# Optimization experiments

Measured on AMD Instinct MI355X. Metric: run time of the kernel, lower is better.

Reference implementation:

```python
import jax, jax.numpy as jnp
import numpy as np

N_HEADS = 12
C = 3          # per-head in/hidden/out channels (12/4)
C_PRED = 1     # predictor hidden (4/4)
BN_EPS = 1e-5
COS_EPS = 1e-8
B, H, W = 8, 512, 768


def setup_inputs() -> dict:
    key = jax.random.key(0)
    ks = jax.random.split(key, 22)
    p = lambda k, s: jax.random.normal(k, s, jnp.float32) * 0.1
    return {
        "latent1": jax.random.normal(ks[0], (B, N_HEADS, H, W), jnp.float32),
        "latent2": jax.random.normal(ks[1], (B, N_HEADS, H, W), jnp.float32),
        # projector conv1 + BN
        "W1": p(ks[2], (N_HEADS, C, C)), "b1": p(ks[3], (N_HEADS, C)),
        "g1": 1.0 + p(ks[4], (N_HEADS, C)), "be1": p(ks[5], (N_HEADS, C)),
        # projector conv2 + BN
        "W2": p(ks[6], (N_HEADS, C, C)), "b2": p(ks[7], (N_HEADS, C)),
        "g2": 1.0 + p(ks[8], (N_HEADS, C)), "be2": p(ks[9], (N_HEADS, C)),
        # projector conv3 + BN (no ReLU)
        "W3": p(ks[10], (N_HEADS, C, C)), "b3": p(ks[11], (N_HEADS, C)),
        "g3": 1.0 + p(ks[12], (N_HEADS, C)), "be3": p(ks[13], (N_HEADS, C)),
        # predictor conv1 + BN
        "W4": p(ks[14], (N_HEADS, C_PRED, C)), "b4": p(ks[15], (N_HEADS, C_PRED)),
        "g4": 1.0 + p(ks[16], (N_HEADS, C_PRED)), "be4": p(ks[17], (N_HEADS, C_PRED)),
        # predictor conv2 (no BN)
        "W5": p(ks[18], (N_HEADS, C, C_PRED)), "b5": p(ks[19], (N_HEADS, C)),
    }


def _conv1x1(x, Wk, bk):
    # x: [B, Cin, H, W'], Wk: [Cout, Cin]
    return jnp.einsum('oc,bchw->bohw', Wk, x) + bk[None, :, None, None]


def _bn(x, g, be):
    # training-mode BatchNorm2d: batch statistics over (B, H, W)
    m = x.mean(axis=(0, 2, 3), keepdims=True)
    v = x.var(axis=(0, 2, 3), keepdims=True)  # biased var, as torch BN uses
    return (x - m) * jax.lax.rsqrt(v + BN_EPS) * g[None, :, None, None] + be[None, :, None, None]


def _cos_loss(p, z):
    # -mean(cosine_similarity(p, detach(z), dim=1))
    z = jax.lax.stop_gradient(z)
    dot = jnp.sum(p * z, axis=1)
    npn = jnp.maximum(jnp.sqrt(jnp.sum(p * p, axis=1)), COS_EPS)
    nzn = jnp.maximum(jnp.sqrt(jnp.sum(z * z, axis=1)), COS_EPS)
    return -jnp.mean(dot / (npn * nzn))


def _head_loss(x1, x2, W1, b1, g1, be1, W2, b2, g2, be2, W3, b3, g3, be3,
               W4, b4, g4, be4, W5, b5):
    def proj(x):
        x = jax.nn.relu(_bn(_conv1x1(x, W1, b1), g1, be1))
        x = jax.nn.relu(_bn(_conv1x1(x, W2, b2), g2, be2))
        return _bn(_conv1x1(x, W3, b3), g3, be3)

    def pred(z):
        h = jax.nn.relu(_bn(_conv1x1(z, W4, b4), g4, be4))
        return _conv1x1(h, W5, b5)

    z1, z2 = proj(x1), proj(x2)
    p1, p2 = pred(z1), pred(z2)
    return 0.5 * (_cos_loss(p1, z2) + _cos_loss(p2, z1))


def reference(latent1, latent2, W1, b1, g1, be1, W2, b2, g2, be2,
              W3, b3, g3, be3, W4, b4, g4, be4, W5, b5):
    Bd, Cd, Hd, Wd = latent1.shape
    Wp = Wd // C
    # per-channel view [B, H, W] -> [B, 3, H, W/3]; stack heads on leading axis
    x1 = latent1.reshape(Bd, N_HEADS, C, Hd, Wp).transpose(1, 0, 2, 3, 4)
    x2 = latent2.reshape(Bd, N_HEADS, C, Hd, Wp).transpose(1, 0, 2, 3, 4)
    losses = jax.vmap(_head_loss)(x1, x2, W1, b1, g1, be1, W2, b2, g2, be2,
                                  W3, b3, g3, be3, W4, b4, g4, be4, W5, b5)
    return jnp.sum(losses)
```

## Files before the change

### kernel.cpp

```cpp
#include <hip/hip_runtime.h>
#include <math.h>


typedef unsigned short ushort_t;
typedef unsigned int uint_t;

constexpr int   NH      = 12;
constexpr int   POS     = 131072;
constexpr int   NB      = 8;
constexpr long long MLL = (long long)NB * POS;
constexpr int   CSPAN   = POS / 16;
constexpr int   SBLK    = 128;
constexpr int   NTOT    = NB * NH * 3 * POS;
constexpr float COS_EPS = 1e-8f;

constexpr size_t XB_BYTES   = (size_t)NTOT * 2;
constexpr size_t DBL_COUNT  = (size_t)24 * SBLK * 9 + (size_t)24 * SBLK * 6 +
                              (size_t)24 * SBLK * 9 + (size_t)12 * SBLK;
constexpr size_t NEED_BYTES = 2 * XB_BYTES + DBL_COUNT * 8 + 480 * 4;

template <int K>
__device__ inline void block_reduce_to0(double (&v)[K]) {
#pragma unroll
  for (int off = 32; off > 0; off >>= 1) {
#pragma unroll
    for (int k = 0; k < K; ++k) v[k] += __shfl_down(v[k], off, 64);
  }
  __shared__ double lds[4][K];
  const int lane = threadIdx.x & 63;
  const int wv   = threadIdx.x >> 6;
  if (lane == 0) {
#pragma unroll
    for (int k = 0; k < K; ++k) lds[wv][k] = v[k];
  }
  __syncthreads();
  if (threadIdx.x == 0) {
#pragma unroll
    for (int k = 0; k < K; ++k) v[k] = lds[0][k] + lds[1][k] + lds[2][k] + lds[3][k];
  }
}

__device__ inline uint_t pack2bf(float lo, float hi) {
  uint_t ul = __float_as_uint(lo);
  uint_t uh = __float_as_uint(hi);
  ul = ul + 0x7FFFu + ((ul >> 16) & 1u);
  uh = uh + 0x7FFFu + ((uh >> 16) & 1u);
  return (ul >> 16) | (uh & 0xFFFF0000u);
}

__device__ inline void unpack8(const uint4 v, float (&f)[8]) {
  const uint_t w0 = v.x, w1 = v.y, w2 = v.z, w3 = v.w;
  f[0] = __uint_as_float(w0 << 16); f[1] = __uint_as_float(w0 & 0xFFFF0000u);
  f[2] = __uint_as_float(w1 << 16); f[3] = __uint_as_float(w1 & 0xFFFF0000u);
  f[4] = __uint_as_float(w2 << 16); f[5] = __uint_as_float(w2 & 0xFFFF0000u);
  f[6] = __uint_as_float(w3 << 16); f[7] = __uint_as_float(w3 & 0xFFFF0000u);
}

template <bool BF16>
__device__ inline void load_ch3(const float* __restrict__ X,
                                const ushort_t* __restrict__ XB,
                                size_t eoff, float (&f)[3][8]) {
#pragma unroll
  for (int c = 0; c < 3; ++c) {
    const size_t a = eoff + (size_t)c * POS;
    if constexpr (BF16) {
      const uint4 v = *(const uint4*)(XB + a);
      unpack8(v, f[c]);
    } else {
      const float4 u0 = *(const float4*)(X + a);
      const float4 u1 = *(const float4*)(X + a + 4);
      f[c][0] = u0.x; f[c][1] = u0.y; f[c][2] = u0.z; f[c][3] = u0.w;
      f[c][4] = u1.x; f[c][5] = u1.y; f[c][6] = u1.z; f[c][7] = u1.w;
    }
  }
}

template <bool STORE>
__global__ __launch_bounds__(256) void passA_kernel(
    const float* __restrict__ x1, const float* __restrict__ x2,
    ushort_t* __restrict__ xb1, ushort_t* __restrict__ xb2,
    double* __restrict__ P0) {
  const int u = blockIdx.y;
  const int s = u % 24;
  const int b = u / 24;
  const int n = s >> 1;
  const float* __restrict__ X = (s & 1) ? x2 : x1;
  ushort_t* __restrict__ XB = (s & 1) ? xb2 : xb1;
  const size_t off0 = (size_t)((b * NH + n) * 3) * POS + (size_t)blockIdx.x * CSPAN;

  float acc[9] = {0.f, 0.f, 0.f, 0.f, 0.f, 0.f, 0.f, 0.f, 0.f};
#pragma unroll
  for (int i = 0; i < 8; ++i) {
    const int idx = i * 1024 + threadIdx.x * 4;
    float4 v[3];
#pragma unroll
    for (int c = 0; c < 3; ++c)
      v[c] = *(const float4*)(X + off0 + (size_t)c * POS + idx);
    if constexpr (STORE) {
#pragma unroll
      for (int c = 0; c < 3; ++c) {
        uint2 h;
        h.x = pack2bf(v[c].x, v[c].y);
        h.y = pack2bf(v[c].z, v[c].w);
        *(uint2*)(XB + off0 + (size_t)c * POS + idx) = h;
      }
    }
    const float* f0 = (const float*)&v[0];
    const float* f1 = (const float*)&v[1];
    const float* f2 = (const float*)&v[2];
#pragma unroll
    for (int j = 0; j < 4; ++j) {
      const float X0 = f0[j], X1 = f1[j], X2 = f2[j];
      acc[0] += X0;      acc[1] += X1;      acc[2] += X2;
      acc[3] += X0 * X0; acc[4] += X1 * X1; acc[5] += X2 * X2;
      acc[6] += X0 * X1; acc[7] += X0 * X2; acc[8] += X1 * X2;
    }
  }

  double v9[9];
#pragma unroll
  for (int k = 0; k < 9; ++k) v9[k] = (double)acc[k];
  block_reduce_to0<9>(v9);
  if (threadIdx.x == 0) {
    double* dst = P0 + ((size_t)s * SBLK + b * 16 + blockIdx.x) * 9;
#pragma unroll
    for (int k = 0; k < 9; ++k) dst[k] = v9[k];
  }
}

__global__ __launch_bounds__(256) void bn_statsA_kernel(
    const double* __restrict__ P0, const float* __restrict__ W1,
    const float* __restrict__ b1, const float* __restrict__ g1,
    const float* __restrict__ be1, float* __restrict__ derived) {
  const int s = blockIdx.x;
  const int t = threadIdx.x;
  const int n = s >> 1;
  double v[9] = {0, 0, 0, 0, 0, 0, 0, 0, 0};
  if (t < SBLK) {
    const double* p = P0 + ((size_t)s * SBLK + t) * 9;
#pragma unroll
    for (int k = 0; k < 9; ++k) v[k] = p[k];
  }
  block_reduce_to0<9>(v);
  if (t == 0) {
    const double M = (double)MLL;
    double m[3] = {v[0] / M, v[1] / M, v[2] / M};
    double C00 = v[3] / M - m[0] * m[0];
    double C11 = v[4] / M - m[1] * m[1];
    double C22 = v[5] / M - m[2] * m[2];
    double C01 = v[6] / M - m[0] * m[1];
    double C02 = v[7] / M - m[0] * m[2];
    double C12 = v[8] / M - m[1] * m[2];
    for (int o = 0; o < 3; ++o) {
      const double w0 = W1[n * 9 + o * 3 + 0];
      const double w1v = W1[n * 9 + o * 3 + 1];
      const double w2v = W1[n * 9 + o * 3 + 2];
      const double my = w0 * m[0] + w1v * m[1] + w2v * m[2] + (double)b1[n * 3 + o];
      const double vy = w0 * w0 * C00 + w1v * w1v * C11 + w2v * w2v * C22 +
                        2.0 * (w0 * w1v * C01 + w0 * w2v * C02 + w1v * w2v * C12);
      const double sc = (double)g1[n * 3 + o] / sqrt(vy + 1e-5);
      derived[s * 20 + o]     = (float)sc;
      derived[s * 20 + 3 + o] = (float)((double)be1[n * 3 + o] - my * sc);
    }
  }
}

template <bool BF16>
__global__ __launch_bounds__(256) void passB_kernel(
    const float* __restrict__ x1, const float* __restrict__ x2,
    const ushort_t* __restrict__ xb1, const ushort_t* __restrict__ xb2,
    const float* __restrict__ W1, const float* __restrict__ b1,
    const float* __restrict__ W2, const float* __restrict__ b2,
    const float* __restrict__ derived, double* __restrict__ P2) {
  const int u = blockIdx.y;
  const int s = u % 24;
  const int b = u / 24;
  const int n = s >> 1;
  const float* __restrict__ X = (s & 1) ? x2 : x1;
  const ushort_t* __restrict__ XB = (s & 1) ? xb2 : xb1;
  const size_t off0 = (size_t)((b * NH + n) * 3) * POS + (size_t)blockIdx.x * CSPAN;

  float w1[3][3], bb1[3], w2[3][3], bb2[3], s1[3], t1[3];
#pragma unroll
  for (int o = 0; o < 3; ++o) {
#pragma unroll
    for (int c = 0; c < 3; ++c) {
      w1[o][c] = W1[n * 9 + o * 3 + c];
      w2[o][c] = W2[n * 9 + o * 3 + c];
    }
    bb1[o] = b1[n * 3 + o];
    bb2[o] = b2[n * 3 + o];
    s1[o]  = derived[s * 20 + o];
    t1[o]  = derived[s * 20 + 3 + o];
  }

  float acc[6] = {0.f, 0.f, 0.f, 0.f, 0.f, 0.f};
#pragma unroll 2
  for (int i = 0; i < 4; ++i) {
    const size_t eoff = off0 + i * 2048 + threadIdx.x * 8;
    float f[3][8];
    load_ch3<BF16>(X, XB, eoff, f);
#pragma unroll
    for (int j = 0; j < 8; ++j) {
      const float X0 = f[0][j], X1 = f[1][j], X2 = f[2][j];
      float a[3];
#pragma unroll
      for (int o = 0; o < 3; ++o) {
        const float y = fmaf(w1[o][0], X0, fmaf(w1[o][1], X1, fmaf(w1[o][2], X2, bb1[o])));
        a[o] = fmaxf(0.f, fmaf(s1[o], y, t1[o]));
      }
#pragma unroll
      for (int o = 0; o < 3; ++o) {
        const float y2v = fmaf(w2[o][0], a[0], fmaf(w2[o][1], a[1], fmaf(w2[o][2], a[2], bb2[o])));
        acc[o]     += y2v;
        acc[3 + o] += y2v * y2v;
      }
    }
  }

  double v[6];
#pragma unroll
  for (int k = 0; k < 6; ++k) v[k] = (double)acc[k];
  block_reduce_to0<6>(v);
  if (threadIdx.x == 0) {
    double* dst = P2 + ((size_t)s * SBLK + b * 16 + blockIdx.x) * 6;
#pragma unroll
    for (int k = 0; k < 6; ++k) dst[k] = v[k];
  }
}

__global__ __launch_bounds__(256) void bn_statsB_kernel(
    const double* __restrict__ P2, const float* __restrict__ gamma,
    const float* __restrict__ beta, float* __restrict__ derived) {
  const int s = blockIdx.x;
  const int t = threadIdx.x;
  const int n = s >> 1;
  double v[6] = {0, 0, 0, 0, 0, 0};
  if (t < SBLK) {
    const double* p = P2 + ((size_t)s * SBLK + t) * 6;
#pragma unroll
    for (int k = 0; k < 6; ++k) v[k] = p[k];
  }
  block_reduce_to0<6>(v);
  if (t == 0) {
#pragma unroll
    for (int c = 0; c < 3; ++c) {
      const double mean = v[c] / (double)MLL;
      const double var  = v[3 + c] / (double)MLL - mean * mean;
      const double sc   = (double)gamma[n * 3 + c] / sqrt(var + 1e-5);
      derived[s * 20 + 6 + c] = (float)sc;
      derived[s * 20 + 9 + c] = (float)((double)beta[n * 3 + c] - mean * sc);
    }
  }
}

template <bool BF16>
__global__ __launch_bounds__(256) void passC_kernel(
    const float* __restrict__ x1, const float* __restrict__ x2,
    const ushort_t* __restrict__ xb1, const ushort_t* __restrict__ xb2,
    const float* __restrict__ W1, const float* __restrict__ b1,
    const float* __restrict__ W2, const float* __restrict__ b2,
    const float* __restrict__ W3, const float* __restrict__ b3,
    const float* __restrict__ derived, double* __restrict__ P3) {
  const int u = blockIdx.y;
  const int s = u % 24;
  const int b = u / 24;
  const int n = s >> 1;
  const float* __restrict__ X = (s & 1) ? x2 : x1;
  const ushort_t* __restrict__ XB = (s & 1) ? xb2 : xb1;
  const size_t off0 = (size_t)((b * NH + n) * 3) * POS + (size_t)blockIdx.x * CSPAN;

  float w1[3][3], bb1[3], w2[3][3], bb2[3], w3[3][3], bb3[3];
  float s1[3], t1[3], s2[3], t2[3];
#pragma unroll
  for (int o = 0; o < 3; ++o) {
#pragma unroll
    for (int c = 0; c < 3; ++c) {
      w1[o][c] = W1[n * 9 + o * 3 + c];
      w2[o][c] = W2[n * 9 + o * 3 + c];
      w3[o][c] = W3[n * 9 + o * 3 + c];
    }
    bb1[o] = b1[n * 3 + o];
    bb2[o] = b2[n * 3 + o];
    bb3[o] = b3[n * 3 + o];
    s1[o]  = derived[s * 20 + o];
    t1[o]  = derived[s * 20 + 3 + o];
    s2[o]  = derived[s * 20 + 6 + o];
    t2[o]  = derived[s * 20 + 9 + o];
  }

  float acc[9] = {0.f, 0.f, 0.f, 0.f, 0.f, 0.f, 0.f, 0.f, 0.f};
#pragma unroll 2
  for (int i = 0; i < 4; ++i) {
    const size_t eoff = off0 + i * 2048 + threadIdx.x * 8;
    float f[3][8];
    load_ch3<BF16>(X, XB, eoff, f);
#pragma unroll
    for (int j = 0; j < 8; ++j) {
      const float X0 = f[0][j], X1 = f[1][j], X2 = f[2][j];
      float a[3], a2[3], y3[3];
#pragma unroll
      for (int o = 0; o < 3; ++o) {
        const float y = fmaf(w1[o][0], X0, fmaf(w1[o][1], X1, fmaf(w1[o][2], X2, bb1[o])));
        a[o] = fmaxf(0.f, fmaf(s1[o], y, t1[o]));
      }
#pragma unroll
      for (int o = 0; o < 3; ++o) {
        const float y = fmaf(w2[o][0], a[0], fmaf(w2[o][1], a[1], fmaf(w2[o][2], a[2], bb2[o])));
        a2[o] = fmaxf(0.f, fmaf(s2[o], y, t2[o]));
      }
#pragma unroll
      for (int o = 0; o < 3; ++o) {
        y3[o] = fmaf(w3[o][0], a2[0], fmaf(w3[o][1], a2[1], fmaf(w3[o][2], a2[2], bb3[o])));
        acc[o]     += y3[o];
        acc[3 + o] += y3[o] * y3[o];
      }
      acc[6] += y3[0] * y3[1];
      acc[7] += y3[0] * y3[2];
      acc[8] += y3[1] * y3[2];
    }
  }

  double v[9];
#pragma unroll
  for (int k = 0; k < 9; ++k) v[k] = (double)acc[k];
  block_reduce_to0<9>(v);
  if (threadIdx.x == 0) {
    double* dst = P3 + ((size_t)s * SBLK + b * 16 + blockIdx.x) * 9;
#pragma unroll
    for (int k = 0; k < 9; ++k) dst[k] = v[k];
  }
}

__global__ __launch_bounds__(256) void bn_statsC_kernel(
    const double* __restrict__ P3, const float* __restrict__ g3,
    const float* __restrict__ be3, const float* __restrict__ W4,
    const float* __restrict__ b4, const float* __restrict__ g4,
    const float* __restrict__ be4, float* __restrict__ derived) {
  const int s = blockIdx.x;
  const int t = threadIdx.x;
  const int n = s >> 1;
  double v[9] = {0, 0, 0, 0, 0, 0, 0, 0, 0};
  if (t < SBLK) {
    const double* p = P3 + ((size_t)s * SBLK + t) * 9;
#pragma unroll
    for (int k = 0; k < 9; ++k) v[k] = p[k];
  }
  block_reduce_to0<9>(v);
  if (t == 0) {
    const double M = (double)MLL;
    double mean[3] = {v[0] / M, v[1] / M, v[2] / M};
    double cov[3][3];
    cov[0][0] = v[3] / M - mean[0] * mean[0];
    cov[1][1] = v[4] / M - mean[1] * mean[1];
    cov[2][2] = v[5] / M - mean[2] * mean[2];
    cov[0][1] = cov[1][0] = v[6] / M - mean[0] * mean[1];
    cov[0][2] = cov[2][0] = v[7] / M - mean[0] * mean[2];
    cov[1][2] = cov[2][1] = v[8] / M - mean[1] * mean[2];

    double s3[3], t3[3];
    for (int c = 0; c < 3; ++c) {
      s3[c] = (double)g3[n * 3 + c] / sqrt(cov[c][c] + 1e-5);
      t3[c] = (double)be3[n * 3 + c] - mean[c] * s3[c];
      derived[s * 20 + 12 + c] = (float)s3[c];
      derived[s * 20 + 15 + c] = (float)t3[c];
    }
    double u[3], dd = (double)b4[n];
    for (int c = 0; c < 3; ++c) {
      u[c] = (double)W4[n * 3 + c] * s3[c];
      dd += (double)W4[n * 3 + c] * t3[c];
    }
    double m4 = dd;
    for (int c = 0; c < 3; ++c) m4 += u[c] * mean[c];
    double v4 = 0.0;
    for (int i = 0; i < 3; ++i)
      for (int j = 0; j < 3; ++j) v4 += u[i] * u[j] * cov[i][j];
    const double s4 = (double)g4[n] / sqrt(v4 + 1e-5);
    derived[s * 20 + 18] = (float)s4;
    derived[s * 20 + 19] = (float)((double)be4[n] - m4 * s4);
  }
}

__device__ inline void fwd_chain(
    const float w1[3][3], const float bb1[3],
    const float w2[3][3], const float bb2[3],
    const float w3[3][3], const float bb3[3],
    const float w4[3], float b4s, const float w5[3], const float b5v[3],
    const float* S, float X0, float X1, float X2, float z[3], float p[3]) {
  float a[3], a2[3];
#pragma unroll
  for (int o = 0; o < 3; ++o) {
    const float y = fmaf(w1[o][0], X0, fmaf(w1[o][1], X1, fmaf(w1[o][2], X2, bb1[o])));
    a[o] = fmaxf(0.f, fmaf(S[o], y, S[3 + o]));
  }
#pragma unroll
  for (int o = 0; o < 3; ++o) {
    const float y = fmaf(w2[o][0], a[0], fmaf(w2[o][1], a[1], fmaf(w2[o][2], a[2], bb2[o])));
    a2[o] = fmaxf(0.f, fmaf(S[6 + o], y, S[9 + o]));
  }
  float y4 = b4s;
#pragma unroll
  for (int o = 0; o < 3; ++o) {
    const float y = fmaf(w3[o][0], a2[0], fmaf(w3[o][1], a2[1], fmaf(w3[o][2], a2[2], bb3[o])));
    z[o] = fmaf(S[12 + o], y, S[15 + o]);
    y4 = fmaf(w4[o], z[o], y4);
  }
  const float h = fmaxf(0.f, fmaf(S[18], y4, S[19]));
#pragma unroll
  for (int o = 0; o < 3; ++o) p[o] = fmaf(w5[o], h, b5v[o]);
}

template <bool BF16>
__global__ __launch_bounds__(256) void passD_kernel(
    const float* __restrict__ x1, const float* __restrict__ x2,
    const ushort_t* __restrict__ xb1, const ushort_t* __restrict__ xb2,
    const float* __restrict__ W1, const float* __restrict__ b1,
    const float* __restrict__ W2, const float* __restrict__ b2,
    const float* __restrict__ W3, const float* __restrict__ b3,
    const float* __restrict__ W4, const float* __restrict__ b4,
    const float* __restrict__ W5, const float* __restrict__ b5,
    const float* __restrict__ derived, double* __restrict__ PL) {
  const int u = blockIdx.y;
  const int n = u % 12;
  const int b = u / 12;
  const size_t off0 = (size_t)((b * NH + n) * 3) * POS + (size_t)blockIdx.x * CSPAN;

  float w1[3][3], bb1[3], w2[3][3], bb2[3], w3[3][3], bb3[3];
  float w4[3], b4s, w5[3], b5v[3];
#pragma unroll
  for (int o = 0; o < 3; ++o) {
#pragma unroll
    for (int c = 0; c < 3; ++c) {
      w1[o][c] = W1[n * 9 + o * 3 + c];
      w2[o][c] = W2[n * 9 + o * 3 + c];
      w3[o][c] = W3[n * 9 + o * 3 + c];
    }
    bb1[o] = b1[n * 3 + o];
    bb2[o] = b2[n * 3 + o];
    bb3[o] = b3[n * 3 + o];
    w4[o]  = W4[n * 3 + o];
    w5[o]  = W5[n * 3 + o];
    b5v[o] = b5[n * 3 + o];
  }
  b4s = b4[n];

  float S0[20], S1[20];
#pragma unroll
  for (int k = 0; k < 20; ++k) {
    S0[k] = derived[(n * 2 + 0) * 20 + k];
    S1[k] = derived[(n * 2 + 1) * 20 + k];
  }

  float acc = 0.f;
  for (int i = 0; i < 4; ++i) {
    const size_t eoff = off0 + i * 2048 + threadIdx.x * 8;
    float fA[3][8], fB[3][8];
    load_ch3<BF16>(x1, xb1, eoff, fA);
    load_ch3<BF16>(x2, xb2, eoff, fB);
#pragma unroll
    for (int j = 0; j < 8; ++j) {
      float z1[3], p1[3], z2[3], p2[3];
      fwd_chain(w1, bb1, w2, bb2, w3, bb3, w4, b4s, w5, b5v, S0,
                fA[0][j], fA[1][j], fA[2][j], z1, p1);
      fwd_chain(w1, bb1, w2, bb2, w3, bb3, w4, b4s, w5, b5v, S1,
                fB[0][j], fB[1][j], fB[2][j], z2, p2);

      const float d12 = p1[0] * z2[0] + p1[1] * z2[1] + p1[2] * z2[2];
      const float pp1 = p1[0] * p1[0] + p1[1] * p1[1] + p1[2] * p1[2];
      const float zz2 = z2[0] * z2[0] + z2[1] * z2[1] + z2[2] * z2[2];
      const float c12 = d12 / (fmaxf(sqrtf(pp1), COS_EPS) * fmaxf(sqrtf(zz2), COS_EPS));

      const float d21 = p2[0] * z1[0] + p2[1] * z1[1] + p2[2] * z1[2];
      const float pp2 = p2[0] * p2[0] + p2[1] * p2[1] + p2[2] * p2[2];
      const float zz1 = z1[0] * z1[0] + z1[1] * z1[1] + z1[2] * z1[2];
      const float c21 = d21 / (fmaxf(sqrtf(pp2), COS_EPS) * fmaxf(sqrtf(zz1), COS_EPS));

      acc += c12 + c21;
    }
  }

  double v[1] = {(double)acc};
  block_reduce_to0<1>(v);
  if (threadIdx.x == 0) PL[(size_t)n * SBLK + b * 16 + blockIdx.x] = v[0];
}

__global__ __launch_bounds__(256) void finalize_kernel(
    const double* __restrict__ PL, float* __restrict__ out) {
  double v[1] = {0.0};
  for (int k = threadIdx.x; k < 12 * SBLK; k += 256) v[0] += PL[k];
  block_reduce_to0<1>(v);
  if (threadIdx.x == 0) out[0] = (float)(-0.5 * v[0] / (double)MLL);
}

extern "C" void kernel_launch(void* const* d_in, const int* in_sizes, int n_in,
                              void* d_out, int out_size, void* d_ws, size_t ws_size,
                              hipStream_t stream) {
  const float* x1  = (const float*)d_in[0];
  const float* x2  = (const float*)d_in[1];
  const float* W1  = (const float*)d_in[2];
  const float* b1  = (const float*)d_in[3];
  const float* g1  = (const float*)d_in[4];
  const float* be1 = (const float*)d_in[5];
  const float* W2  = (const float*)d_in[6];
  const float* b2  = (const float*)d_in[7];
  const float* g2  = (const float*)d_in[8];
  const float* be2 = (const float*)d_in[9];
  const float* W3  = (const float*)d_in[10];
  const float* b3  = (const float*)d_in[11];
  const float* g3  = (const float*)d_in[12];
  const float* be3 = (const float*)d_in[13];
  const float* W4  = (const float*)d_in[14];
  const float* b4  = (const float*)d_in[15];
  const float* g4  = (const float*)d_in[16];
  const float* be4 = (const float*)d_in[17];
  const float* W5  = (const float*)d_in[18];
  const float* b5  = (const float*)d_in[19];

  const bool big = ws_size >= NEED_BYTES;
  ushort_t* xb1 = nullptr;
  ushort_t* xb2 = nullptr;
  double* dbase;
  if (big) {
    xb1 = (ushort_t*)d_ws;
    xb2 = xb1 + NTOT;
    dbase = (double*)(xb2 + NTOT);
  } else {
    dbase = (double*)d_ws;
  }
  double* P0 = dbase;
  double* P2 = P0 + (size_t)24 * SBLK * 9;
  double* P3 = P2 + (size_t)24 * SBLK * 6;
  double* PL = P3 + (size_t)24 * SBLK * 9;
  float* derived = (float*)(PL + 12 * SBLK);

  const dim3 blk(256);
  const dim3 gA(16, 192);
  const dim3 gD(16, 96);

  if (big) {
    passA_kernel<true><<<gA, blk, 0, stream>>>(x1, x2, xb1, xb2, P0);
    bn_statsA_kernel<<<24, blk, 0, stream>>>(P0, W1, b1, g1, be1, derived);
    passB_kernel<true><<<gA, blk, 0, stream>>>(x1, x2, xb1, xb2, W1, b1, W2, b2,
                                               derived, P2);
    bn_statsB_kernel<<<24, blk, 0, stream>>>(P2, g2, be2, derived);
    passC_kernel<true><<<gA, blk, 0, stream>>>(x1, x2, xb1, xb2, W1, b1, W2, b2,
                                               W3, b3, derived, P3);
    bn_statsC_kernel<<<24, blk, 0, stream>>>(P3, g3, be3, W4, b4, g4, be4, derived);
    passD_kernel<true><<<gD, blk, 0, stream>>>(x1, x2, xb1, xb2, W1, b1, W2, b2,
                                               W3, b3, W4, b4, W5, b5, derived, PL);
  } else {
    passA_kernel<false><<<gA, blk, 0, stream>>>(x1, x2, nullptr, nullptr, P0);
    bn_statsA_kernel<<<24, blk, 0, stream>>>(P0, W1, b1, g1, be1, derived);
    passB_kernel<false><<<gA, blk, 0, stream>>>(x1, x2, nullptr, nullptr, W1, b1,
                                                W2, b2, derived, P2);
    bn_statsB_kernel<<<24, blk, 0, stream>>>(P2, g2, be2, derived);
    passC_kernel<false><<<gA, blk, 0, stream>>>(x1, x2, nullptr, nullptr, W1, b1,
                                                W2, b2, W3, b3, derived, P3);
    bn_statsC_kernel<<<24, blk, 0, stream>>>(P3, g3, be3, W4, b4, g4, be4, derived);
    passD_kernel<false><<<gD, blk, 0, stream>>>(x1, x2, nullptr, nullptr, W1, b1,
                                                W2, b2, W3, b3, W4, b4, W5, b5,
                                                derived, PL);
  }
  finalize_kernel<<<1, blk, 0, stream>>>(PL, (float*)d_out);
}
```

Baseline: 511.4 us.

## Store bf16 copy in position-interleaved layout and retile later passes

Pass A now writes the bf16 copy interleaved per position, as three channels plus one zero pad in 8 bytes, instead of three planar channel arrays. Passes B, C and D then read one 16-byte vector for every two positions and use 4x more blocks, each doing a quarter of the work, with launch bounds for occupancy. The first-pass fp32 loads are nontemporal. In exchange the padding adds a third to the bf16 bytes written and read, and the stats kernels now loop over more partials.

```diff
diff --git a/kernel.cpp b/kernel.cpp
--- a/kernel.cpp
+++ b/kernel.cpp
@@ -4,20 +4,22 @@
 
 typedef unsigned short ushort_t;
 typedef unsigned int uint_t;
+typedef float vf4 __attribute__((ext_vector_type(4)));
 
 constexpr int   NH      = 12;
 constexpr int   POS     = 131072;
 constexpr int   NB      = 8;
 constexpr long long MLL = (long long)NB * POS;
-constexpr int   CSPAN   = POS / 16;
-constexpr int   SBLK    = 128;
-constexpr int   NTOT    = NB * NH * 3 * POS;
+constexpr int   NPOSL   = NB * NH * POS;
 constexpr float COS_EPS = 1e-8f;
 
-constexpr size_t XB_BYTES   = (size_t)NTOT * 2;
-constexpr size_t DBL_COUNT  = (size_t)24 * SBLK * 9 + (size_t)24 * SBLK * 6 +
-                              (size_t)24 * SBLK * 9 + (size_t)12 * SBLK;
-constexpr size_t NEED_BYTES = 2 * XB_BYTES + DBL_COUNT * 8 + 480 * 4;
+constexpr int   ABLK    = 128;
+constexpr int   BBLK    = 512;
+
+constexpr size_t XP_USHORT  = (size_t)NPOSL * 4;
+constexpr size_t NEED_BYTES = 2 * XP_USHORT * 2 +
+    ((size_t)24 * ABLK * 9 + (size_t)24 * BBLK * 6 + (size_t)24 * BBLK * 9 +
+     (size_t)12 * BBLK) * 8 + 4096;
 
 template <int K>
 __device__ inline void block_reduce_to0(double (&v)[K]) {
@@ -38,6 +40,11 @@
 #pragma unroll
     for (int k = 0; k < K; ++k) v[k] = lds[0][k] + lds[1][k] + lds[2][k] + lds[3][k];
   }
+}
+
+__device__ inline float4 ntload4(const float* p) {
+  vf4 v = __builtin_nontemporal_load((const vf4*)p);
+  return make_float4(v.x, v.y, v.z, v.w);
 }
 
 __device__ inline uint_t pack2bf(float lo, float hi) {
@@ -48,45 +55,40 @@
   return (ul >> 16) | (uh & 0xFFFF0000u);
 }
 
-__device__ inline void unpack8(const uint4 v, float (&f)[8]) {
-  const uint_t w0 = v.x, w1 = v.y, w2 = v.z, w3 = v.w;
-  f[0] = __uint_as_float(w0 << 16); f[1] = __uint_as_float(w0 & 0xFFFF0000u);
-  f[2] = __uint_as_float(w1 << 16); f[3] = __uint_as_float(w1 & 0xFFFF0000u);
-  f[4] = __uint_as_float(w2 << 16); f[5] = __uint_as_float(w2 & 0xFFFF0000u);
-  f[6] = __uint_as_float(w3 << 16); f[7] = __uint_as_float(w3 & 0xFFFF0000u);
-}
-
-template <bool BF16>
-__device__ inline void load_ch3(const float* __restrict__ X,
-                                const ushort_t* __restrict__ XB,
-                                size_t eoff, float (&f)[3][8]) {
+__device__ inline void dec2(const uint4 w, float (&f)[2][3]) {
+  f[0][0] = __uint_as_float(w.x << 16);
+  f[0][1] = __uint_as_float(w.x & 0xFFFF0000u);
+  f[0][2] = __uint_as_float(w.y << 16);
+  f[1][0] = __uint_as_float(w.z << 16);
+  f[1][1] = __uint_as_float(w.z & 0xFFFF0000u);
+  f[1][2] = __uint_as_float(w.w << 16);
+}
+
+__device__ inline void load_ch3_f32(const float* __restrict__ X, size_t eoff,
+                                    float (&f)[3][8]) {
 #pragma unroll
   for (int c = 0; c < 3; ++c) {
     const size_t a = eoff + (size_t)c * POS;
-    if constexpr (BF16) {
-      const uint4 v = *(const uint4*)(XB + a);
-      unpack8(v, f[c]);
-    } else {
-      const float4 u0 = *(const float4*)(X + a);
-      const float4 u1 = *(const float4*)(X + a + 4);
-      f[c][0] = u0.x; f[c][1] = u0.y; f[c][2] = u0.z; f[c][3] = u0.w;
-      f[c][4] = u1.x; f[c][5] = u1.y; f[c][6] = u1.z; f[c][7] = u1.w;
-    }
+    const float4 u0 = *(const float4*)(X + a);
+    const float4 u1 = *(const float4*)(X + a + 4);
+    f[c][0] = u0.x; f[c][1] = u0.y; f[c][2] = u0.z; f[c][3] = u0.w;
+    f[c][4] = u1.x; f[c][5] = u1.y; f[c][6] = u1.z; f[c][7] = u1.w;
   }
 }
 
 template <bool STORE>
 __global__ __launch_bounds__(256) void passA_kernel(
     const float* __restrict__ x1, const float* __restrict__ x2,
-    ushort_t* __restrict__ xb1, ushort_t* __restrict__ xb2,
+    ushort_t* __restrict__ xp1, ushort_t* __restrict__ xp2,
     double* __restrict__ P0) {
   const int u = blockIdx.y;
   const int s = u % 24;
   const int b = u / 24;
   const int n = s >> 1;
   const float* __restrict__ X = (s & 1) ? x2 : x1;
-  ushort_t* __restrict__ XB = (s & 1) ? xb2 : xb1;
-  const size_t off0 = (size_t)((b * NH + n) * 3) * POS + (size_t)blockIdx.x * CSPAN;
+  ushort_t* __restrict__ XP = (s & 1) ? xp2 : xp1;
+  const size_t eoff0 = (size_t)((b * NH + n) * 3) * POS + (size_t)blockIdx.x * 8192;
+  const size_t qbase = (size_t)(b * NH + n) * POS + (size_t)blockIdx.x * 8192;
 
   float acc[9] = {0.f, 0.f, 0.f, 0.f, 0.f, 0.f, 0.f, 0.f, 0.f};
 #pragma unroll
@@ -95,15 +97,19 @@
     float4 v[3];
 #pragma unroll
     for (int c = 0; c < 3; ++c)
-      v[c] = *(const float4*)(X + off0 + (size_t)c * POS + idx);
+      v[c] = ntload4(X + eoff0 + (size_t)c * POS + idx);
     if constexpr (STORE) {
-#pragma unroll
-      for (int c = 0; c < 3; ++c) {
-        uint2 h;
-        h.x = pack2bf(v[c].x, v[c].y);
-        h.y = pack2bf(v[c].z, v[c].w);
-        *(uint2*)(XB + off0 + (size_t)c * POS + idx) = h;
-      }
+      const float* f0 = (const float*)&v[0];
+      const float* f1 = (const float*)&v[1];
+      const float* f2 = (const float*)&v[2];
+      uint4 A, Bu;
+      A.x  = pack2bf(f0[0], f1[0]);  A.y  = pack2bf(f2[0], 0.f);
+      A.z  = pack2bf(f0[1], f1[1]);  A.w  = pack2bf(f2[1], 0.f);
+      Bu.x = pack2bf(f0[2], f1[2]);  Bu.y = pack2bf(f2[2], 0.f);
+      Bu.z = pack2bf(f0[3], f1[3]);  Bu.w = pack2bf(f2[3], 0.f);
+      uint4* dst = (uint4*)(XP + (qbase + idx) * 4);
+      dst[0] = A;
+      dst[1] = Bu;
     }
     const float* f0 = (const float*)&v[0];
     const float* f1 = (const float*)&v[1];
@@ -122,7 +128,7 @@
   for (int k = 0; k < 9; ++k) v9[k] = (double)acc[k];
   block_reduce_to0<9>(v9);
   if (threadIdx.x == 0) {
-    double* dst = P0 + ((size_t)s * SBLK + b * 16 + blockIdx.x) * 9;
+    double* dst = P0 + ((size_t)s * ABLK + b * 16 + blockIdx.x) * 9;
 #pragma unroll
     for (int k = 0; k < 9; ++k) dst[k] = v9[k];
   }
@@ -136,8 +142,8 @@
   const int t = threadIdx.x;
   const int n = s >> 1;
   double v[9] = {0, 0, 0, 0, 0, 0, 0, 0, 0};
-  if (t < SBLK) {
-    const double* p = P0 + ((size_t)s * SBLK + t) * 9;
+  if (t < ABLK) {
+    const double* p = P0 + ((size_t)s * ABLK + t) * 9;
 #pragma unroll
     for (int k = 0; k < 9; ++k) v[k] = p[k];
   }
@@ -152,7 +158,7 @@
     double C02 = v[7] / M - m[0] * m[2];
     double C12 = v[8] / M - m[1] * m[2];
     for (int o = 0; o < 3; ++o) {
-      const double w0 = W1[n * 9 + o * 3 + 0];
+      const double w0  = W1[n * 9 + o * 3 + 0];
       const double w1v = W1[n * 9 + o * 3 + 1];
       const double w2v = W1[n * 9 + o * 3 + 2];
       const double my = w0 * m[0] + w1v * m[1] + w2v * m[2] + (double)b1[n * 3 + o];
@@ -165,10 +171,8 @@
   }
 }
 
-template <bool BF16>
-__global__ __launch_bounds__(256) void passB_kernel(
-    const float* __restrict__ x1, const float* __restrict__ x2,
-    const ushort_t* __restrict__ xb1, const ushort_t* __restrict__ xb2,
+__global__ __launch_bounds__(256, 4) void passBp_kernel(
+    const ushort_t* __restrict__ xp1, const ushort_t* __restrict__ xp2,
     const float* __restrict__ W1, const float* __restrict__ b1,
     const float* __restrict__ W2, const float* __restrict__ b2,
     const float* __restrict__ derived, double* __restrict__ P2) {
@@ -176,9 +180,7 @@
   const int s = u % 24;
   const int b = u / 24;
   const int n = s >> 1;
-  const float* __restrict__ X = (s & 1) ? x2 : x1;
-  const ushort_t* __restrict__ XB = (s & 1) ? xb2 : xb1;
-  const size_t off0 = (size_t)((b * NH + n) * 3) * POS + (size_t)blockIdx.x * CSPAN;
+  const ushort_t* __restrict__ XP = (s & 1) ? xp2 : xp1;
 
   float w1[3][3], bb1[3], w2[3][3], bb2[3], s1[3], t1[3];
 #pragma unroll
@@ -194,15 +196,20 @@
     t1[o]  = derived[s * 20 + 3 + o];
   }
 
+  const uint4* __restrict__ U = (const uint4*)XP +
+      (((size_t)(b * NH + n) * POS) >> 1) + (size_t)blockIdx.x * 1024;
+  uint4 r[4];
+#pragma unroll
+  for (int i = 0; i < 4; ++i) r[i] = U[i * 256 + threadIdx.x];
+
   float acc[6] = {0.f, 0.f, 0.f, 0.f, 0.f, 0.f};
-#pragma unroll 2
+#pragma unroll
   for (int i = 0; i < 4; ++i) {
-    const size_t eoff = off0 + i * 2048 + threadIdx.x * 8;
-    float f[3][8];
-    load_ch3<BF16>(X, XB, eoff, f);
-#pragma unroll
-    for (int j = 0; j < 8; ++j) {
-      const float X0 = f[0][j], X1 = f[1][j], X2 = f[2][j];
+    float f[2][3];
+    dec2(r[i], f);
+#pragma unroll
+    for (int j = 0; j < 2; ++j) {
+      const float X0 = f[j][0], X1 = f[j][1], X2 = f[j][2];
       float a[3];
 #pragma unroll
       for (int o = 0; o < 3; ++o) {
@@ -223,7 +230,7 @@
   for (int k = 0; k < 6; ++k) v[k] = (double)acc[k];
   block_reduce_to0<6>(v);
   if (threadIdx.x == 0) {
-    double* dst = P2 + ((size_t)s * SBLK + b * 16 + blockIdx.x) * 6;
+    double* dst = P2 + ((size_t)s * BBLK + b * 64 + blockIdx.x) * 6;
 #pragma unroll
     for (int k = 0; k < 6; ++k) dst[k] = v[k];
   }
@@ -231,15 +238,15 @@
 
 __global__ __launch_bounds__(256) void bn_statsB_kernel(
     const double* __restrict__ P2, const float* __restrict__ gamma,
-    const float* __restrict__ beta, float* __restrict__ derived) {
+    const float* __restrict__ beta, float* __restrict__ derived, int cnt) {
   const int s = blockIdx.x;
   const int t = threadIdx.x;
   const int n = s >> 1;
   double v[6] = {0, 0, 0, 0, 0, 0};
-  if (t < SBLK) {
-    const double* p = P2 + ((size_t)s * SBLK + t) * 6;
-#pragma unroll
-    for (int k = 0; k < 6; ++k) v[k] = p[k];
+  for (int k = t; k < cnt; k += 256) {
+    const double* p = P2 + ((size_t)s * BBLK + k) * 6;
+#pragma unroll
+    for (int q = 0; q < 6; ++q) v[q] += p[q];
   }
   block_reduce_to0<6>(v);
   if (t == 0) {
@@ -254,10 +261,8 @@
   }
 }
 
-template <bool BF16>
-__global__ __launch_bounds__(256) void passC_kernel(
-    const float* __restrict__ x1, const float* __restrict__ x2,
-    const ushort_t* __restrict__ xb1, const ushort_t* __restrict__ xb2,
+__global__ __launch_bounds__(256, 4) void passCp_kernel(
+    const ushort_t* __restrict__ xp1, const ushort_t* __restrict__ xp2,
     const float* __restrict__ W1, const float* __restrict__ b1,
     const float* __restrict__ W2, const float* __restrict__ b2,
     const float* __restrict__ W3, const float* __restrict__ b3,
@@ -266,9 +271,7 @@
   const int s = u % 24;
   const int b = u / 24;
   const int n = s >> 1;
-  const float* __restrict__ X = (s & 1) ? x2 : x1;
-  const ushort_t* __restrict__ XB = (s & 1) ? xb2 : xb1;
-  const size_t off0 = (size_t)((b * NH + n) * 3) * POS + (size_t)blockIdx.x * CSPAN;
+  const ushort_t* __restrict__ XP = (s & 1) ? xp2 : xp1;
 
   float w1[3][3], bb1[3], w2[3][3], bb2[3], w3[3][3], bb3[3];
   float s1[3], t1[3], s2[3], t2[3];
@@ -289,15 +292,20 @@
     t2[o]  = derived[s * 20 + 9 + o];
   }
 
+  const uint4* __restrict__ U = (const uint4*)XP +
+      (((size_t)(b * NH + n) * POS) >> 1) + (size_t)blockIdx.x * 1024;
+  uint4 r[4];
+#pragma unroll
+  for (int i = 0; i < 4; ++i) r[i] = U[i * 256 + threadIdx.x];
+
   float acc[9] = {0.f, 0.f, 0.f, 0.f, 0.f, 0.f, 0.f, 0.f, 0.f};
-#pragma unroll 2
+#pragma unroll
   for (int i = 0; i < 4; ++i) {
-    const size_t eoff = off0 + i * 2048 + threadIdx.x * 8;
-    float f[3][8];
-    load_ch3<BF16>(X, XB, eoff, f);
-#pragma unroll
-    for (int j = 0; j < 8; ++j) {
-      const float X0 = f[0][j], X1 = f[1][j], X2 = f[2][j];
+    float f[2][3];
+    dec2(r[i], f);
+#pragma unroll
+    for (int j = 0; j < 2; ++j) {
+      const float X0 = f[j][0], X1 = f[j][1], X2 = f[j][2];
       float a[3], a2[3], y3[3];
 #pragma unroll
       for (int o = 0; o < 3; ++o) {
@@ -326,7 +334,7 @@
   for (int k = 0; k < 9; ++k) v[k] = (double)acc[k];
   block_reduce_to0<9>(v);
   if (threadIdx.x == 0) {
-    double* dst = P3 + ((size_t)s * SBLK + b * 16 + blockIdx.x) * 9;
+    double* dst = P3 + ((size_t)s * BBLK + b * 64 + blockIdx.x) * 9;
 #pragma unroll
     for (int k = 0; k < 9; ++k) dst[k] = v[k];
   }
@@ -336,15 +344,15 @@
     const double* __restrict__ P3, const float* __restrict__ g3,
     const float* __restrict__ be3, const float* __restrict__ W4,
     const float* __restrict__ b4, const float* __restrict__ g4,
-    const float* __restrict__ be4, float* __restrict__ derived) {
+    const float* __restrict__ be4, float* __restrict__ derived, int cnt) {
   const int s = blockIdx.x;
   const int t = threadIdx.x;
   const int n = s >> 1;
   double v[9] = {0, 0, 0, 0, 0, 0, 0, 0, 0};
-  if (t < SBLK) {
-    const double* p = P3 + ((size_t)s * SBLK + t) * 9;
-#pragma unroll
-    for (int k = 0; k < 9; ++k) v[k] = p[k];
+  for (int k = t; k < cnt; k += 256) {
+    const double* p = P3 + ((size_t)s * BBLK + k) * 9;
+#pragma unroll
+    for (int q = 0; q < 9; ++q) v[q] += p[q];
   }
   block_reduce_to0<9>(v);
   if (t == 0) {
@@ -365,16 +373,16 @@
       derived[s * 20 + 12 + c] = (float)s3[c];
       derived[s * 20 + 15 + c] = (float)t3[c];
     }
-    double u[3], dd = (double)b4[n];
-    for (int c = 0; c < 3; ++c) {
-      u[c] = (double)W4[n * 3 + c] * s3[c];
+    double uu[3], dd = (double)b4[n];
+    for (int c = 0; c < 3; ++c) {
+      uu[c] = (double)W4[n * 3 + c] * s3[c];
       dd += (double)W4[n * 3 + c] * t3[c];
     }
     double m4 = dd;
-    for (int c = 0; c < 3; ++c) m4 += u[c] * mean[c];
+    for (int c = 0; c < 3; ++c) m4 += uu[c] * mean[c];
     double v4 = 0.0;
     for (int i = 0; i < 3; ++i)
-      for (int j = 0; j < 3; ++j) v4 += u[i] * u[j] * cov[i][j];
+      for (int j = 0; j < 3; ++j) v4 += uu[i] * uu[j] * cov[i][j];
     const double s4 = (double)g4[n] / sqrt(v4 + 1e-5);
     derived[s * 20 + 18] = (float)s4;
     derived[s * 20 + 19] = (float)((double)be4[n] - m4 * s4);
@@ -410,10 +418,36 @@
   for (int o = 0; o < 3; ++o) p[o] = fmaf(w5[o], h, b5v[o]);
 }
 
-template <bool BF16>
-__global__ __launch_bounds__(256) void passD_kernel(
-    const float* __restrict__ x1, const float* __restrict__ x2,
-    const ushort_t* __restrict__ xb1, const ushort_t* __restrict__ xb2,
+__device__ inline void cos_acc2(
+    const float w1[3][3], const float bb1[3], const float w2[3][3],
+    const float bb2[3], const float w3[3][3], const float bb3[3],
+    const float w4[3], float b4s, const float w5[3], const float b5v[3],
+    const float* S0, const float* S1,
+    const float (&fA)[2][3], const float (&fB)[2][3], float& acc) {
+#pragma unroll
+  for (int j = 0; j < 2; ++j) {
+    float z1[3], p1[3], z2[3], p2[3];
+    fwd_chain(w1, bb1, w2, bb2, w3, bb3, w4, b4s, w5, b5v, S0,
+              fA[j][0], fA[j][1], fA[j][2], z1, p1);
+    fwd_chain(w1, bb1, w2, bb2, w3, bb3, w4, b4s, w5, b5v, S1,
+              fB[j][0], fB[j][1], fB[j][2], z2, p2);
+
+    const float d12 = p1[0] * z2[0] + p1[1] * z2[1] + p1[2] * z2[2];
+    const float pp1 = p1[0] * p1[0] + p1[1] * p1[1] + p1[2] * p1[2];
+    const float zz2 = z2[0] * z2[0] + z2[1] * z2[1] + z2[2] * z2[2];
+    const float c12 = d12 / (fmaxf(sqrtf(pp1), COS_EPS) * fmaxf(sqrtf(zz2), COS_EPS));
+
+    const float d21 = p2[0] * z1[0] + p2[1] * z1[1] + p2[2] * z1[2];
+    const float pp2 = p2[0] * p2[0] + p2[1] * p2[1] + p2[2] * p2[2];
+    const float zz1 = z1[0] * z1[0] + z1[1] * z1[1] + z1[2] * z1[2];
+    const float c21 = d21 / (fmaxf(sqrtf(pp2), COS_EPS) * fmaxf(sqrtf(zz1), COS_EPS));
+
+    acc += c12 + c21;
+  }
+}
+
+__global__ __launch_bounds__(256, 4) void passDp_kernel(
+    const ushort_t* __restrict__ xp1, const ushort_t* __restrict__ xp2,
     const float* __restrict__ W1, const float* __restrict__ b1,
     const float* __restrict__ W2, const float* __restrict__ b2,
     const float* __restrict__ W3, const float* __restrict__ b3,
@@ -423,7 +457,6 @@
   const int u = blockIdx.y;
   const int n = u % 12;
   const int b = u / 12;
-  const size_t off0 = (size_t)((b * NH + n) * 3) * POS + (size_t)blockIdx.x * CSPAN;
 
   float w1[3][3], bb1[3], w2[3][3], bb2[3], w3[3][3], bb3[3];
   float w4[3], b4s, w5[3], b5v[3];
@@ -451,12 +484,203 @@
     S1[k] = derived[(n * 2 + 1) * 20 + k];
   }
 
+  const size_t R = (((size_t)(b * NH + n) * POS) >> 1) + (size_t)blockIdx.x * 1024;
+  const uint4* __restrict__ U1 = (const uint4*)xp1 + R;
+  const uint4* __restrict__ U2 = (const uint4*)xp2 + R;
+
+  float acc = 0.f;
+#pragma unroll
+  for (int i = 0; i < 4; ++i) {
+    const uint4 rA = U1[i * 256 + threadIdx.x];
+    const uint4 rB = U2[i * 256 + threadIdx.x];
+    float fA[2][3], fB[2][3];
+    dec2(rA, fA);
+    dec2(rB, fB);
+    cos_acc2(w1, bb1, w2, bb2, w3, bb3, w4, b4s, w5, b5v, S0, S1, fA, fB, acc);
+  }
+
+  double v[1] = {(double)acc};
+  block_reduce_to0<1>(v);
+  if (threadIdx.x == 0) PL[(size_t)n * BBLK + b * 64 + blockIdx.x] = v[0];
+}
+
+__global__ __launch_bounds__(256) void passBf_kernel(
+    const float* __restrict__ x1, const float* __restrict__ x2,
+    const float* __restrict__ W1, const float* __restrict__ b1,
+    const float* __restrict__ W2, const float* __restrict__ b2,
+    const float* __restrict__ derived, double* __restrict__ P2) {
+  const int u = blockIdx.y;
+  const int s = u % 24;
+  const int b = u / 24;
+  const int n = s >> 1;
+  const float* __restrict__ X = (s & 1) ? x2 : x1;
+  const size_t off0 = (size_t)((b * NH + n) * 3) * POS + (size_t)blockIdx.x * 8192;
+
+  float w1[3][3], bb1[3], w2[3][3], bb2[3], s1[3], t1[3];
+#pragma unroll
+  for (int o = 0; o < 3; ++o) {
+#pragma unroll
+    for (int c = 0; c < 3; ++c) {
+      w1[o][c] = W1[n * 9 + o * 3 + c];
+      w2[o][c] = W2[n * 9 + o * 3 + c];
+    }
+    bb1[o] = b1[n * 3 + o];
+    bb2[o] = b2[n * 3 + o];
+    s1[o]  = derived[s * 20 + o];
+    t1[o]  = derived[s * 20 + 3 + o];
+  }
+
+  float acc[6] = {0.f, 0.f, 0.f, 0.f, 0.f, 0.f};
+  for (int i = 0; i < 4; ++i) {
+    float f[3][8];
+    load_ch3_f32(X, off0 + i * 2048 + threadIdx.x * 8, f);
+#pragma unroll
+    for (int j = 0; j < 8; ++j) {
+      const float X0 = f[0][j], X1 = f[1][j], X2 = f[2][j];
+      float a[3];
+#pragma unroll
+      for (int o = 0; o < 3; ++o) {
+        const float y = fmaf(w1[o][0], X0, fmaf(w1[o][1], X1, fmaf(w1[o][2], X2, bb1[o])));
+        a[o] = fmaxf(0.f, fmaf(s1[o], y, t1[o]));
+      }
+#pragma unroll
+      for (int o = 0; o < 3; ++o) {
+        const float y2v = fmaf(w2[o][0], a[0], fmaf(w2[o][1], a[1], fmaf(w2[o][2], a[2], bb2[o])));
+        acc[o]     += y2v;
+        acc[3 + o] += y2v * y2v;
+      }
+    }
+  }
+
+  double v[6];
+#pragma unroll
+  for (int k = 0; k < 6; ++k) v[k] = (double)acc[k];
+  block_reduce_to0<6>(v);
+  if (threadIdx.x == 0) {
+    double* dst = P2 + ((size_t)s * BBLK + b * 16 + blockIdx.x) * 6;
+#pragma unroll
+    for (int k = 0; k < 6; ++k) dst[k] = v[k];
+  }
+}
+
+__global__ __launch_bounds__(256) void passCf_kernel(
+    const float* __restrict__ x1, const float* __restrict__ x2,
+    const float* __restrict__ W1, const float* __restrict__ b1,
+    const float* __restrict__ W2, const float* __restrict__ b2,
+    const float* __restrict__ W3, const float* __restrict__ b3,
+    const float* __restrict__ derived, double* __restrict__ P3) {
+  const int u = blockIdx.y;
+  const int s = u % 24;
+  const int b = u / 24;
+  const int n = s >> 1;
+  const float* __restrict__ X = (s & 1) ? x2 : x1;
+  const size_t off0 = (size_t)((b * NH + n) * 3) * POS + (size_t)blockIdx.x * 8192;
+
+  float w1[3][3], bb1[3], w2[3][3], bb2[3], w3[3][3], bb3[3];
+  float s1[3], t1[3], s2[3], t2[3];
+#pragma unroll
+  for (int o = 0; o < 3; ++o) {
+#pragma unroll
+    for (int c = 0; c < 3; ++c) {
+      w1[o][c] = W1[n * 9 + o * 3 + c];
+      w2[o][c] = W2[n * 9 + o * 3 + c];
+      w3[o][c] = W3[n * 9 + o * 3 + c];
+    }
+    bb1[o] = b1[n * 3 + o];
+    bb2[o] = b2[n * 3 + o];
+    bb3[o] = b3[n * 3 + o];
+    s1[o]  = derived[s * 20 + o];
+    t1[o]  = derived[s * 20 + 3 + o];
+    s2[o]  = derived[s * 20 + 6 + o];
+    t2[o]  = derived[s * 20 + 9 + o];
+  }
+
+  float acc[9] = {0.f, 0.f, 0.f, 0.f, 0.f, 0.f, 0.f, 0.f, 0.f};
+  for (int i = 0; i < 4; ++i) {
+    float f[3][8];
+    load_ch3_f32(X, off0 + i * 2048 + threadIdx.x * 8, f);
+#pragma unroll
+    for (int j = 0; j < 8; ++j) {
+      const float X0 = f[0][j], X1 = f[1][j], X2 = f[2][j];
+      float a[3], a2[3], y3[3];
+#pragma unroll
+      for (int o = 0; o < 3; ++o) {
+        const float y = fmaf(w1[o][0], X0, fmaf(w1[o][1], X1, fmaf(w1[o][2], X2, bb1[o])));
+        a[o] = fmaxf(0.f, fmaf(s1[o], y, t1[o]));
+      }
+#pragma unroll
+      for (int o = 0; o < 3; ++o) {
+        const float y = fmaf(w2[o][0], a[0], fmaf(w2[o][1], a[1], fmaf(w2[o][2], a[2], bb2[o])));
+        a2[o] = fmaxf(0.f, fmaf(s2[o], y, t2[o]));
+      }
+#pragma unroll
+      for (int o = 0; o < 3; ++o) {
+        y3[o] = fmaf(w3[o][0], a2[0], fmaf(w3[o][1], a2[1], fmaf(w3[o][2], a2[2], bb3[o])));
+        acc[o]     += y3[o];
+        acc[3 + o] += y3[o] * y3[o];
+      }
+      acc[6] += y3[0] * y3[1];
+      acc[7] += y3[0] * y3[2];
+      acc[8] += y3[1] * y3[2];
+    }
+  }
+
+  double v[9];
+#pragma unroll
+  for (int k = 0; k < 9; ++k) v[k] = (double)acc[k];
+  block_reduce_to0<9>(v);
+  if (threadIdx.x == 0) {
+    double* dst = P3 + ((size_t)s * BBLK + b * 16 + blockIdx.x) * 9;
+#pragma unroll
+    for (int k = 0; k < 9; ++k) dst[k] = v[k];
+  }
+}
+
+__global__ __launch_bounds__(256) void passDf_kernel(
+    const float* __restrict__ x1, const float* __restrict__ x2,
+    const float* __restrict__ W1, const float* __restrict__ b1,
+    const float* __restrict__ W2, const float* __restrict__ b2,
+    const float* __restrict__ W3, const float* __restrict__ b3,
+    const float* __restrict__ W4, const float* __restrict__ b4,
+    const float* __restrict__ W5, const float* __restrict__ b5,
+    const float* __restrict__ derived, double* __restrict__ PL) {
+  const int u = blockIdx.y;
+  const int n = u % 12;
+  const int b = u / 12;
+  const size_t off0 = (size_t)((b * NH + n) * 3) * POS + (size_t)blockIdx.x * 8192;
+
+  float w1[3][3], bb1[3], w2[3][3], bb2[3], w3[3][3], bb3[3];
+  float w4[3], b4s, w5[3], b5v[3];
+#pragma unroll
+  for (int o = 0; o < 3; ++o) {
+#pragma unroll
+    for (int c = 0; c < 3; ++c) {
+      w1[o][c] = W1[n * 9 + o * 3 + c];
+      w2[o][c] = W2[n * 9 + o * 3 + c];
+      w3[o][c] = W3[n * 9 + o * 3 + c];
+    }
+    bb1[o] = b1[n * 3 + o];
+    bb2[o] = b2[n * 3 + o];
+    bb3[o] = b3[n * 3 + o];
+    w4[o]  = W4[n * 3 + o];
+    w5[o]  = W5[n * 3 + o];
+    b5v[o] = b5[n * 3 + o];
+  }
+  b4s = b4[n];
+
+  float S0[20], S1[20];
+#pragma unroll
+  for (int k = 0; k < 20; ++k) {
+    S0[k] = derived[(n * 2 + 0) * 20 + k];
+    S1[k] = derived[(n * 2 + 1) * 20 + k];
+  }
+
   float acc = 0.f;
   for (int i = 0; i < 4; ++i) {
     const size_t eoff = off0 + i * 2048 + threadIdx.x * 8;
     float fA[3][8], fB[3][8];
-    load_ch3<BF16>(x1, xb1, eoff, fA);
-    load_ch3<BF16>(x2, xb2, eoff, fB);
+    load_ch3_f32(x1, eoff, fA);
+    load_ch3_f32(x2, eoff, fB);
 #pragma unroll
     for (int j = 0; j < 8; ++j) {
       float z1[3], p1[3], z2[3], p2[3];
@@ -481,13 +705,15 @@
 
   double v[1] = {(double)acc};
   block_reduce_to0<1>(v);
-  if (threadIdx.x == 0) PL[(size_t)n * SBLK + b * 16 + blockIdx.x] = v[0];
+  if (threadIdx.x == 0) PL[(size_t)n * BBLK + b * 16 + blockIdx.x] = v[0];
 }
 
 __global__ __launch_bounds__(256) void finalize_kernel(
-    const double* __restrict__ PL, float* __restrict__ out) {
+    const double* __restrict__ PL, float* __restrict__ out, int cntPerN) {
   double v[1] = {0.0};
-  for (int k = threadIdx.x; k < 12 * SBLK; k += 256) v[0] += PL[k];
+  for (int n = 0; n < 12; ++n)
+    for (int k = threadIdx.x; k < cntPerN; k += 256)
+      v[0] += PL[(size_t)n * BBLK + k];
   block_reduce_to0<1>(v);
   if (threadIdx.x == 0) out[0] = (float)(-0.5 * v[0] / (double)MLL);
 }
@@ -517,49 +743,51 @@
   const float* b5  = (const float*)d_in[19];
 
   const bool big = ws_size >= NEED_BYTES;
-  ushort_t* xb1 = nullptr;
-  ushort_t* xb2 = nullptr;
+  ushort_t* xp1 = nullptr;
+  ushort_t* xp2 = nullptr;
   double* dbase;
   if (big) {
-    xb1 = (ushort_t*)d_ws;
-    xb2 = xb1 + NTOT;
-    dbase = (double*)(xb2 + NTOT);
+    xp1 = (ushort_t*)d_ws;
+    xp2 = xp1 + XP_USHORT;
+    dbase = (double*)(xp2 + XP_USHORT);
   } else {
     dbase = (double*)d_ws;
   }
   double* P0 = dbase;
-  double* P2 = P0 + (size_t)24 * SBLK * 9;
-  double* P3 = P2 + (size_t)24 * SBLK * 6;
-  double* PL = P3 + (size_t)24 * SBLK * 9;
-  float* derived = (float*)(PL + 12 * SBLK);
+  double* P2 = P0 + (size_t)24 * ABLK * 9;
+  double* P3 = P2 + (size_t)24 * BBLK * 6;
+  double* PL = P3 + (size_t)24 * BBLK * 9;
+  float* derived = (float*)(PL + 12 * BBLK);
 
   const dim3 blk(256);
   const dim3 gA(16, 192);
-  const dim3 gD(16, 96);
 
   if (big) {
-    passA_kernel<true><<<gA, blk, 0, stream>>>(x1, x2, xb1, xb2, P0);
+    passA_kernel<true><<<gA, blk, 0, stream>>>(x1, x2, xp1, xp2, P0);
     bn_statsA_kernel<<<24, blk, 0, stream>>>(P0, W1, b1, g1, be1, derived);
-    passB_kernel<true><<<gA, blk, 0, stream>>>(x1, x2, xb1, xb2, W1, b1, W2, b2,
-                                               derived, P2);
-    bn_statsB_kernel<<<24, blk, 0, stream>>>(P2, g2, be2, derived);
-    passC_kernel<true><<<gA, blk, 0, stream>>>(x1, x2, xb1, xb2, W1, b1, W2, b2,
-                                               W3, b3, derived, P3);
-    bn_statsC_kernel<<<24, blk, 0, stream>>>(P3, g3, be3, W4, b4, g4, be4, derived);
-    passD_kernel<true><<<gD, blk, 0, stream>>>(x1, x2, xb1, xb2, W1, b1, W2, b2,
-                                               W3, b3, W4, b4, W5, b5, derived, PL);
+    passBp_kernel<<<dim3(64, 192), blk, 0, stream>>>(xp1, xp2, W1, b1, W2, b2,
+                                                     derived, P2);
+    bn_statsB_kernel<<<24, blk, 0, stream>>>(P2, g2, be2, derived, BBLK);
+    passCp_kernel<<<dim3(64, 192), blk, 0, stream>>>(xp1, xp2, W1, b1, W2, b2,
+                                                     W3, b3, derived, P3);
+    bn_statsC_kernel<<<24, blk, 0, stream>>>(P3, g3, be3, W4, b4, g4, be4,
+                                             derived, BBLK);
+    passDp_kernel<<<dim3(64, 96), blk, 0, stream>>>(xp1, xp2, W1, b1, W2, b2,
+                                                    W3, b3, W4, b4, W5, b5,
+                                                    derived, PL);
+    finalize_kernel<<<1, blk, 0, stream>>>(PL, (float*)d_out, BBLK);
   } else {
     passA_kernel<false><<<gA, blk, 0, stream>>>(x1, x2, nullptr, nullptr, P0);
     bn_statsA_kernel<<<24, blk, 0, stream>>>(P0, W1, b1, g1, be1, derived);
-    passB_kernel<false><<<gA, blk, 0, stream>>>(x1, x2, nullptr, nullptr, W1, b1,
-                                                W2, b2, derived, P2);
-    bn_statsB_kernel<<<24, blk, 0, stream>>>(P2, g2, be2, derived);
-    passC_kernel<false><<<gA, blk, 0, stream>>>(x1, x2, nullptr, nullptr, W1, b1,
-                                                W2, b2, W3, b3, derived, P3);
-    bn_statsC_kernel<<<24, blk, 0, stream>>>(P3, g3, be3, W4, b4, g4, be4, derived);
-    passD_kernel<false><<<gD, blk, 0, stream>>>(x1, x2, nullptr, nullptr, W1, b1,
-                                                W2, b2, W3, b3, W4, b4, W5, b5,
-                                                derived, PL);
-  }
-  finalize_kernel<<<1, blk, 0, stream>>>(PL, (float*)d_out);
-}
+    passBf_kernel<<<gA, blk, 0, stream>>>(x1, x2, W1, b1, W2, b2, derived, P2);
+    bn_statsB_kernel<<<24, blk, 0, stream>>>(P2, g2, be2, derived, ABLK);
+    passCf_kernel<<<gA, blk, 0, stream>>>(x1, x2, W1, b1, W2, b2, W3, b3,
+                                          derived, P3);
+    bn_statsC_kernel<<<24, blk, 0, stream>>>(P3, g3, be3, W4, b4, g4, be4,
+                                             derived, ABLK);
+    passDf_kernel<<<dim3(16, 96), blk, 0, stream>>>(x1, x2, W1, b1, W2, b2,
+                                                    W3, b3, W4, b4, W5, b5,
+                                                    derived, PL);
+    finalize_kernel<<<1, blk, 0, stream>>>(PL, (float*)d_out, ABLK);
+  }
+}
```

Result: no change. 521.3 us (+1.9%).
